# Kernel optimization log

Hardware: AMD Instinct MI355X
Metric: run time of the kernel (lower is better)

## Reference

```python
import jax, jax.numpy as jnp
import numpy as np

D_MODEL = 1024
NUM_HEADS = 16
D_K = D_MODEL // NUM_HEADS
B, S = 4, 2048


def setup_inputs() -> dict:
    key = jax.random.key(0)
    ks = jax.random.split(key, 12)
    scale = 1.0 / np.sqrt(D_MODEL)
    inp = {
        "query": jax.random.normal(ks[0], (B, S, D_MODEL), jnp.float32),
        "key": jax.random.normal(ks[1], (B, S, D_MODEL), jnp.float32),
        "value": jax.random.normal(ks[2], (B, S, D_MODEL), jnp.float32),
        # causal mask, broadcastable over (batch, heads)
        "mask": jnp.tril(jnp.ones((S, S), jnp.int32))[None, None, :, :],
        "Wq": jax.random.normal(ks[3], (D_MODEL, D_MODEL), jnp.float32) * scale,
        "bq": jnp.zeros((D_MODEL,), jnp.float32),
        "Wk": jax.random.normal(ks[4], (D_MODEL, D_MODEL), jnp.float32) * scale,
        "bk": jnp.zeros((D_MODEL,), jnp.float32),
        "Wv": jax.random.normal(ks[5], (D_MODEL, D_MODEL), jnp.float32) * scale,
        "bv": jnp.zeros((D_MODEL,), jnp.float32),
        "Wo": jax.random.normal(ks[6], (D_MODEL, D_MODEL), jnp.float32) * scale,
        "bo": jnp.zeros((D_MODEL,), jnp.float32),
    }
    return inp


def reference(query, key, value, mask, Wq, bq, Wk, bk, Wv, bv, Wo, bo):
    b = query.shape[0]
    # projections (torch Linear: x @ W.T + b)
    Q = query @ Wq.T + bq
    K = key @ Wk.T + bk
    V = value @ Wv.T + bv
    # [B, S, D] -> [B, H, S, d_k]
    def split_heads(x):
        return x.reshape(b, -1, NUM_HEADS, D_K).transpose(0, 2, 1, 3)
    Q, K, V = split_heads(Q), split_heads(K), split_heads(V)
    # scaled dot-product attention, full score matrix as in original
    scores = jnp.einsum("bhqd,bhkd->bhqk", Q, K) / jnp.sqrt(jnp.float32(D_K))
    scores = jnp.where(mask == 0, jnp.float32(-jnp.inf), scores)
    attn = jax.nn.softmax(scores, axis=-1)  # dropout p=0.0 -> identity
    x = jnp.einsum("bhqk,bhkd->bhqd", attn, V)
    # [B, H, S, d_k] -> [B, S, D]
    x = x.transpose(0, 2, 1, 3).reshape(b, -1, D_MODEL)
    return x @ Wo.T + bo
```

## Files before the change

kernel.cpp:

```cpp
#include <hip/hip_runtime.h>
#include <hip/hip_bf16.h>
#include <stdint.h>

#define D_MODEL 1024
#define NUM_HEADS 16
#define DK 64
#define BATCH 4
#define SEQ 2048
#define MTOT (BATCH * SEQ)

typedef unsigned short u16;
typedef unsigned int u32;
typedef __bf16 bf16x8 __attribute__((ext_vector_type(8)));
typedef float f32x4 __attribute__((ext_vector_type(4)));
typedef short s16x4 __attribute__((ext_vector_type(4)));
typedef int   i32x4 __attribute__((ext_vector_type(4)));
typedef int   i32x2 __attribute__((ext_vector_type(2)));
typedef uint  u32x2 __attribute__((ext_vector_type(2)));

__device__ __forceinline__ f32x4 mfma16(s16x4 a, s16x4 b, f32x4 c) {
  return __builtin_amdgcn_mfma_f32_16x16x16bf16_1k(a, b, c, 0, 0, 0);
}

__device__ __forceinline__ u16 f2bf(float f) {
  union { float f; unsigned u; } c; c.f = f;
  unsigned u = c.u + 0x7fffu + ((c.u >> 16) & 1u);
  return (u16)(u >> 16);
}
__device__ __forceinline__ u32 pack_bf2(float f0, float f1) {
  return __builtin_amdgcn_perm(__float_as_uint(f1), __float_as_uint(f0), 0x07060302u);
}
__device__ __forceinline__ s16x4 cast_s16x4(u32 lo, u32 hi) {
  u32x2 t = {lo, hi};
  return (s16x4)t;
}

__device__ __forceinline__ void async16(void* g, void* lds) {
  __builtin_amdgcn_global_load_lds(
      (__attribute__((address_space(1))) void*)g,
      (__attribute__((address_space(3))) void*)lds,
      16, 0, 0);
}

struct CvtArgs {
  const float* s[7];
  u16* d[7];
  int n[7];
};
__global__ __launch_bounds__(256)
void cvt_multi(CvtArgs a) {
  const int which = blockIdx.y;
  const int n = a.n[which];
  const int i = (blockIdx.x * 256 + threadIdx.x) * 8;
  if (i >= n) return;
  const float* s = a.s[which];
  u16* d = a.d[which];
  const float4 x = *(const float4*)(s + i);
  const float4 y = *(const float4*)(s + i + 4);
  *(ushort4*)(d + i)     = make_ushort4(f2bf(x.x), f2bf(x.y), f2bf(x.z), f2bf(x.w));
  *(ushort4*)(d + i + 4) = make_ushort4(f2bf(y.x), f2bf(y.y), f2bf(y.z), f2bf(y.w));
}

struct GBatch {
  const u16* A[3]; const u16* W[3]; const float* bias[3];
  void* C[3]; float osc[3]; int mode[3];
};
__global__ __launch_bounds__(256, 2)
void gemm_bt_bias(GBatch ga)
{
  __shared__ __align__(16) u16 smem[24576];
  const int z = blockIdx.z;
  const u16* __restrict__ A = ga.A[z];
  const u16* __restrict__ W = ga.W[z];
  const float* __restrict__ bias = ga.bias[z];
  void* __restrict__ Cv = ga.C[z];
  const float oscale = ga.osc[z];
  const int mode = ga.mode[z];

  const int t = threadIdx.x;
  const int w = t >> 6, l = t & 63;
  const int quad = l >> 4, lane16 = l & 15;
  const int m0 = blockIdx.x * 128;
  const int n0 = blockIdx.y * 128;
  const int wm = (w >> 1) * 64, wn = (w & 1) * 64;

  const int srow = t >> 2;
  const int scol = (t & 3) * 8;
  const u16* Ag = A + (long)(m0 + srow) * D_MODEL + scol;
  const u16* Wg = W + (long)(n0 + srow) * D_MODEL + scol;

  f32x4 acc[4][4] = {};

  auto stage = [&](int buf, int k0) {
    u16* As_ = smem + buf * 8192;
    u16* Bs_ = As_ + 4096;
    async16((void*)(Ag + k0), As_ + w * 512);
    async16((void*)(Ag + 64 * D_MODEL + k0), As_ + w * 512 + 2048);
    async16((void*)(Wg + k0), Bs_ + w * 512);
    async16((void*)(Wg + 64 * D_MODEL + k0), Bs_ + w * 512 + 2048);
  };
  auto compute = [&](int buf) {
    const u16* As_ = smem + buf * 8192;
    const u16* Bs_ = As_ + 4096;
    bf16x8 af[4], bfr[4];
#pragma unroll
    for (int i = 0; i < 4; ++i)
      af[i] = *(const bf16x8*)&As_[(wm + i * 16 + lane16) * 32 + quad * 8];
#pragma unroll
    for (int i = 0; i < 4; ++i)
      bfr[i] = *(const bf16x8*)&Bs_[(wn + i * 16 + lane16) * 32 + quad * 8];
#pragma unroll
    for (int i = 0; i < 4; ++i)
#pragma unroll
      for (int jn = 0; jn < 4; ++jn)
        acc[i][jn] = __builtin_amdgcn_mfma_f32_16x16x32_bf16(af[i], bfr[jn], acc[i][jn], 0, 0, 0);
  };

  stage(0, 0);
  stage(1, 32);
  asm volatile("s_waitcnt vmcnt(4)" ::: "memory");
  __builtin_amdgcn_s_barrier();
  __builtin_amdgcn_sched_barrier(0);

  int buf = 0;
#pragma unroll 1
  for (int c = 0; c < 32; ++c) {
    if (c + 2 < 32) stage((buf + 2 >= 3) ? buf - 1 : buf + 2, (c + 2) * 32);
    compute(buf);
    if (c < 30) {
      asm volatile("s_waitcnt vmcnt(4)" ::: "memory");
      __builtin_amdgcn_s_barrier();
      __builtin_amdgcn_sched_barrier(0);
    } else if (c == 30) {
      asm volatile("s_waitcnt vmcnt(0)" ::: "memory");
      __builtin_amdgcn_s_barrier();
      __builtin_amdgcn_sched_barrier(0);
    }
    buf = (buf + 1 == 3) ? 0 : buf + 1;
  }
  __syncthreads();

  if (mode == 1) {
    u16* T = smem;
#pragma unroll
    for (int jn = 0; jn < 4; ++jn) {
      const int col = wn + jn * 16 + lane16;
      const float bb = bias[n0 + col];
#pragma unroll
      for (int i = 0; i < 4; ++i) {
        const int rbase = wm + i * 16 + quad * 4;
#pragma unroll
        for (int r = 0; r < 4; ++r)
          T[col * 132 + rbase + r] = f2bf((acc[i][jn][r] + bb) * oscale);
      }
    }
    __syncthreads();
    const int bq = m0 >> 11, sbase = m0 & 2047;
    const int a = t & 31;
    const int keystart = ((a >> 3) * 32) + (((a & 7) >> 1) * 4) + ((a & 1) * 16);
    u16* orow = (u16*)Cv + ((long)bq * 1024 + n0) * SEQ + sbase + 4 * a;
#pragma unroll
    for (int pass = 0; pass < 16; ++pass) {
      const int dkl = (t >> 5) + 8 * pass;
      *(u32x2*)(orow + (long)dkl * SEQ) = *(const u32x2*)&T[dkl * 132 + keystart];
    }
  } else {
#pragma unroll
    for (int jn = 0; jn < 4; ++jn) {
      const int col = n0 + wn + jn * 16 + lane16;
      const float bb = bias[col];
#pragma unroll
      for (int i = 0; i < 4; ++i) {
        const int rbase = m0 + wm + i * 16 + quad * 4;
#pragma unroll
        for (int r = 0; r < 4; ++r) {
          const float v = (acc[i][jn][r] + bb) * oscale;
          if (mode == 2) ((float*)Cv)[(long)(rbase + r) * D_MODEL + col] = v;
          else           ((u16*)Cv)[(long)(rbase + r) * D_MODEL + col] = f2bf(v);
        }
      }
    }
  }
}

__global__ __launch_bounds__(256, 3)
void attn_causal(const u16* __restrict__ Q, const u16* __restrict__ K,
                 const u16* __restrict__ VtX, u16* __restrict__ O)
{
  __shared__ __align__(16) u16 Kb[2][32][64];
  __shared__ __align__(16) u16 Vb[2][64][32];
  const int t = threadIdx.x;
  const int w = t >> 6, l = t & 63;
  const int quad = l >> 4, lane16 = l & 15;

  const int lin = blockIdx.x;
  const int xcd = lin & 7;
  const int j = lin >> 3;
  const int bh = xcd * 8 + (j & 7);
  const int g = 15 - (j >> 3);
  const int b = bh >> 4, h = bh & 15;
  const int sw = 4 * g + w;
  const int cmax = 4 * g + 3;
  const int qbase = sw * 32;

  const long qkbase = (long)b * SEQ * D_MODEL + h * DK;

  bf16x8 qf[2][2];
#pragma unroll
  for (int qi = 0; qi < 2; ++qi)
#pragma unroll
    for (int ks = 0; ks < 2; ++ks)
      qf[qi][ks] = *(const bf16x8*)&Q[qkbase +
          (long)(qbase + qi * 16 + lane16) * D_MODEL + ks * 32 + quad * 8];

  const int krow = t >> 3, kc = t & 7;
  const char* Kgt = (const char*)(K + qkbase) + (long)krow * (D_MODEL * 2) + kc * 16;
  u16* KbD0 = &Kb[0][krow][(kc ^ (krow & 7)) * 8];
  u16* KbD1 = &Kb[1][krow][(kc ^ (krow & 7)) * 8];
  const int vrow = t >> 2, vc = t & 3;
  const char* Vgt = (const char*)(VtX + ((long)b * 1024 + h * 64) * SEQ) +
                    (long)vrow * (SEQ * 2) + vc * 16;
  u16* VbD0 = &Vb[0][vrow][(vc ^ (vrow & 3)) * 8];
  u16* VbD1 = &Vb[1][vrow][(vc ^ (vrow & 3)) * 8];

  f32x4 oacc[4][2] = {};
  float lsum[2] = {0.f, 0.f};

  auto body = [&](const u16 (*Kbuf)[64], const u16 (*Vbuf)[32], bool diag) {
    bf16x8 kf[2][2];
#pragma unroll
    for (int kt = 0; kt < 2; ++kt)
#pragma unroll
      for (int ks = 0; ks < 2; ++ks)
        kf[kt][ks] = *(const bf16x8*)
            &Kbuf[kt * 16 + lane16][(((ks * 4 + quad) ^ (lane16 & 7)) * 8)];
    i32x4 vfd[4];
#pragma unroll
    for (int d = 0; d < 4; ++d)
      vfd[d] = *(const i32x4*)
          &Vbuf[d * 16 + lane16][((quad ^ (lane16 & 3)) * 8)];

    f32x4 st[2][2] = {};
    __builtin_amdgcn_s_setprio(1);
#pragma unroll
    for (int kt = 0; kt < 2; ++kt)
#pragma unroll
      for (int qi = 0; qi < 2; ++qi)
#pragma unroll
        for (int ks = 0; ks < 2; ++ks)
          st[kt][qi] = __builtin_amdgcn_mfma_f32_16x16x32_bf16(kf[kt][ks], qf[qi][ks], st[kt][qi], 0, 0, 0);
    __builtin_amdgcn_s_setprio(0);

    u32 pb[2][2][2];
#pragma unroll
    for (int kt = 0; kt < 2; ++kt)
#pragma unroll
      for (int qi = 0; qi < 2; ++qi) {
        float pv[4];
#pragma unroll
        for (int r = 0; r < 4; ++r) {
          float p = __builtin_amdgcn_exp2f(st[kt][qi][r]);
          if (diag && (kt * 16 + quad * 4 + r > qi * 16 + lane16)) p = 0.f;
          pv[r] = p;
        }
        lsum[qi] += (pv[0] + pv[1]) + (pv[2] + pv[3]);
        pb[kt][qi][0] = pack_bf2(pv[0], pv[1]);
        pb[kt][qi][1] = pack_bf2(pv[2], pv[3]);
      }

    __builtin_amdgcn_s_setprio(1);
#pragma unroll
    for (int d = 0; d < 4; ++d) {
      const s16x4 va0 = cast_s16x4((u32)vfd[d].x, (u32)vfd[d].y);
      const s16x4 va1 = cast_s16x4((u32)vfd[d].z, (u32)vfd[d].w);
#pragma unroll
      for (int qi = 0; qi < 2; ++qi) {
        const s16x4 pb0 = cast_s16x4(pb[0][qi][0], pb[0][qi][1]);
        const s16x4 pb1 = cast_s16x4(pb[1][qi][0], pb[1][qi][1]);
        oacc[d][qi] = mfma16(va0, pb0, oacc[d][qi]);
        oacc[d][qi] = mfma16(va1, pb1, oacc[d][qi]);
      }
    }
    __builtin_amdgcn_s_setprio(0);
  };

  {
    i32x4 a0 = *(const i32x4*)(Kgt);
    i32x4 a1 = *(const i32x4*)(Vgt);
    *(i32x4*)KbD0 = a0;
    *(i32x4*)VbD0 = a1;
  }
  i32x4 gKA = *(const i32x4*)(Kgt + 65536);
  i32x4 gVA = *(const i32x4*)(Vgt + 64);
  i32x4 gKB = *(const i32x4*)(Kgt + 2 * 65536);
  i32x4 gVB = *(const i32x4*)(Vgt + 2 * 64);
  __syncthreads();

  for (int c = 0; c <= cmax; c += 2) {
    *(i32x4*)KbD1 = gKA;
    *(i32x4*)VbD1 = gVA;
    if (c + 3 <= cmax) {
      gKA = *(const i32x4*)(Kgt + (long)(c + 3) * 65536);
      gVA = *(const i32x4*)(Vgt + (long)(c + 3) * 64);
    }
    if (c <= sw) body(Kb[0], Vb[0], c == sw);
    __syncthreads();
    if (c + 2 <= cmax) {
      *(i32x4*)KbD0 = gKB;
      *(i32x4*)VbD0 = gVB;
      if (c + 4 <= cmax) {
        gKB = *(const i32x4*)(Kgt + (long)(c + 4) * 65536);
        gVB = *(const i32x4*)(Vgt + (long)(c + 4) * 64);
      }
    }
    if (c + 1 <= sw) body(Kb[1], Vb[1], (c + 1) == sw);
    __syncthreads();
  }

  float linv[2];
#pragma unroll
  for (int qi = 0; qi < 2; ++qi) {
    float v = lsum[qi];
    v += __shfl_xor(v, 16);
    v += __shfl_xor(v, 32);
    linv[qi] = 1.f / v;
  }

#pragma unroll
  for (int qi = 0; qi < 2; ++qi) {
    const long row = (long)b * SEQ + qbase + qi * 16 + lane16;
#pragma unroll
    for (int d = 0; d < 4; ++d) {
      const u32 p0 = ((u32)f2bf(oacc[d][qi][0] * linv[qi])) |
                     ((u32)f2bf(oacc[d][qi][1] * linv[qi]) << 16);
      const u32 p1 = ((u32)f2bf(oacc[d][qi][2] * linv[qi])) |
                     ((u32)f2bf(oacc[d][qi][3] * linv[qi]) << 16);
      u32x2 pk = {p0, p1};
      *(u32x2*)&O[row * D_MODEL + h * 64 + d * 16 + quad * 4] = pk;
    }
  }
}

extern "C" void kernel_launch(void* const* d_in, const int* in_sizes, int n_in,
                              void* d_out, int out_size, void* d_ws, size_t ws_size,
                              hipStream_t stream) {
  const float* q  = (const float*)d_in[0];
  const float* k  = (const float*)d_in[1];
  const float* v  = (const float*)d_in[2];
  const float* Wq = (const float*)d_in[4];
  const float* bq = (const float*)d_in[5];
  const float* Wk = (const float*)d_in[6];
  const float* bk = (const float*)d_in[7];
  const float* Wv = (const float*)d_in[8];
  const float* bv = (const float*)d_in[9];
  const float* Wo = (const float*)d_in[10];
  const float* bo = (const float*)d_in[11];
  float* out = (float*)d_out;

  const size_t NT = (size_t)MTOT * D_MODEL;
  const size_t NW = (size_t)D_MODEL * D_MODEL;

  u16* w0  = (u16*)d_ws;
  u16* qb  = w0;
  u16* kb  = w0 + NT;
  u16* vb  = w0 + 2 * NT;
  u16* Wqb = w0 + 3 * NT;
  u16* Wkb = Wqb + NW;
  u16* Wvb = Wqb + 2 * NW;
  u16* Wob = Wqb + 3 * NW;
  u16* Qp  = (u16*)d_out;
  u16* Kp  = (u16*)d_out + NT;
  u16* Vpt = qb;
  u16* Xp  = kb;

  const dim3 blk(256);

  CvtArgs ca;
  ca.s[0] = q;  ca.d[0] = qb;  ca.n[0] = (int)NT;
  ca.s[1] = k;  ca.d[1] = kb;  ca.n[1] = (int)NT;
  ca.s[2] = v;  ca.d[2] = vb;  ca.n[2] = (int)NT;
  ca.s[3] = Wq; ca.d[3] = Wqb; ca.n[3] = (int)NW;
  ca.s[4] = Wk; ca.d[4] = Wkb; ca.n[4] = (int)NW;
  ca.s[5] = Wv; ca.d[5] = Wvb; ca.n[5] = (int)NW;
  ca.s[6] = Wo; ca.d[6] = Wob; ca.n[6] = (int)NW;
  cvt_multi<<<dim3(4096, 7), blk, 0, stream>>>(ca);

  const float SC = 0.125f * 1.4426950408889634f;

  GBatch g1;
  g1.A[0] = qb; g1.W[0] = Wqb; g1.bias[0] = bq; g1.C[0] = Qp;  g1.osc[0] = SC;  g1.mode[0] = 0;
  g1.A[1] = kb; g1.W[1] = Wkb; g1.bias[1] = bk; g1.C[1] = Kp;  g1.osc[1] = 1.f; g1.mode[1] = 0;
  g1.A[2] = vb; g1.W[2] = Wvb; g1.bias[2] = bv; g1.C[2] = Vpt; g1.osc[2] = 1.f; g1.mode[2] = 1;
  gemm_bt_bias<<<dim3(MTOT / 128, D_MODEL / 128, 3), blk, 0, stream>>>(g1);

  const dim3 agrid(1024);
  attn_causal<<<agrid, blk, 0, stream>>>(Qp, Kp, Vpt, Xp);

  GBatch g2;
  for (int i = 0; i < 3; ++i) {
    g2.A[i] = Xp; g2.W[i] = Wob; g2.bias[i] = bo; g2.C[i] = out;
    g2.osc[i] = 1.f; g2.mode[i] = 2;
  }
  gemm_bt_bias<<<dim3(MTOT / 128, D_MODEL / 128, 1), blk, 0, stream>>>(g2);
}
```

Before: 312.3 us.

## Deepen GEMM prefetch to four LDS stages and template epilogue mode

The projection GEMM moves from a 3-buffer to a 4-buffer LDS ring, so three k-chunks are in flight ahead of compute, with the vmcnt waits adjusted to match. The epilogue mode becomes a template parameter so the branch and the per-z argument struct lookups are resolved at compile time. The three Q/K/V projections, previously one batched launch over blockIdx.z, are now split into three separate launches. LDS use per block grows from 48KB to 64KB, which may limit occupancy, and the split launches give up the single large grid plus add launch gaps.

```diff
diff --git a/kernel.cpp b/kernel.cpp
--- a/kernel.cpp
+++ b/kernel.cpp
@@ -61,22 +61,13 @@
   *(ushort4*)(d + i + 4) = make_ushort4(f2bf(y.x), f2bf(y.y), f2bf(y.z), f2bf(y.w));
 }
 
-struct GBatch {
-  const u16* A[3]; const u16* W[3]; const float* bias[3];
-  void* C[3]; float osc[3]; int mode[3];
-};
+template <int MODE>
 __global__ __launch_bounds__(256, 2)
-void gemm_bt_bias(GBatch ga)
+void gemm_bt_bias(const u16* __restrict__ A, const u16* __restrict__ W,
+                  const float* __restrict__ bias, void* __restrict__ Cv,
+                  float oscale)
 {
-  __shared__ __align__(16) u16 smem[24576];
-  const int z = blockIdx.z;
-  const u16* __restrict__ A = ga.A[z];
-  const u16* __restrict__ W = ga.W[z];
-  const float* __restrict__ bias = ga.bias[z];
-  void* __restrict__ Cv = ga.C[z];
-  const float oscale = ga.osc[z];
-  const int mode = ga.mode[z];
-
+  __shared__ __align__(16) u16 smem[32768];
   const int t = threadIdx.x;
   const int w = t >> 6, l = t & 63;
   const int quad = l >> 4, lane16 = l & 15;
@@ -118,29 +109,28 @@
 
   stage(0, 0);
   stage(1, 32);
-  asm volatile("s_waitcnt vmcnt(4)" ::: "memory");
+  stage(2, 64);
+  asm volatile("s_waitcnt vmcnt(8)" ::: "memory");
   __builtin_amdgcn_s_barrier();
   __builtin_amdgcn_sched_barrier(0);
 
   int buf = 0;
 #pragma unroll 1
   for (int c = 0; c < 32; ++c) {
-    if (c + 2 < 32) stage((buf + 2 >= 3) ? buf - 1 : buf + 2, (c + 2) * 32);
+    if (c + 3 < 32) stage((buf + 3) & 3, (c + 3) * 32);
     compute(buf);
-    if (c < 30) {
-      asm volatile("s_waitcnt vmcnt(4)" ::: "memory");
+    if (c < 31) {
+      if (c <= 28)      asm volatile("s_waitcnt vmcnt(8)" ::: "memory");
+      else if (c == 29) asm volatile("s_waitcnt vmcnt(4)" ::: "memory");
+      else              asm volatile("s_waitcnt vmcnt(0)" ::: "memory");
       __builtin_amdgcn_s_barrier();
       __builtin_amdgcn_sched_barrier(0);
-    } else if (c == 30) {
-      asm volatile("s_waitcnt vmcnt(0)" ::: "memory");
-      __builtin_amdgcn_s_barrier();
-      __builtin_amdgcn_sched_barrier(0);
-    }
-    buf = (buf + 1 == 3) ? 0 : buf + 1;
+    }
+    buf = (buf + 1) & 3;
   }
   __syncthreads();
 
-  if (mode == 1) {
+  if constexpr (MODE == 1) {
     u16* T = smem;
 #pragma unroll
     for (int jn = 0; jn < 4; ++jn) {
@@ -175,7 +165,7 @@
 #pragma unroll
         for (int r = 0; r < 4; ++r) {
           const float v = (acc[i][jn][r] + bb) * oscale;
-          if (mode == 2) ((float*)Cv)[(long)(rbase + r) * D_MODEL + col] = v;
+          if (MODE == 2) ((float*)Cv)[(long)(rbase + r) * D_MODEL + col] = v;
           else           ((u16*)Cv)[(long)(rbase + r) * D_MODEL + col] = f2bf(v);
         }
       }
@@ -386,20 +376,14 @@
   cvt_multi<<<dim3(4096, 7), blk, 0, stream>>>(ca);
 
   const float SC = 0.125f * 1.4426950408889634f;
-
-  GBatch g1;
-  g1.A[0] = qb; g1.W[0] = Wqb; g1.bias[0] = bq; g1.C[0] = Qp;  g1.osc[0] = SC;  g1.mode[0] = 0;
-  g1.A[1] = kb; g1.W[1] = Wkb; g1.bias[1] = bk; g1.C[1] = Kp;  g1.osc[1] = 1.f; g1.mode[1] = 0;
-  g1.A[2] = vb; g1.W[2] = Wvb; g1.bias[2] = bv; g1.C[2] = Vpt; g1.osc[2] = 1.f; g1.mode[2] = 1;
-  gemm_bt_bias<<<dim3(MTOT / 128, D_MODEL / 128, 3), blk, 0, stream>>>(g1);
+  const dim3 ggrid(MTOT / 128, D_MODEL / 128);
+
+  gemm_bt_bias<0><<<ggrid, blk, 0, stream>>>(qb, Wqb, bq, Qp,  SC);
+  gemm_bt_bias<0><<<ggrid, blk, 0, stream>>>(kb, Wkb, bk, Kp,  1.f);
+  gemm_bt_bias<1><<<ggrid, blk, 0, stream>>>(vb, Wvb, bv, Vpt, 1.f);
 
   const dim3 agrid(1024);
   attn_causal<<<agrid, blk, 0, stream>>>(Qp, Kp, Vpt, Xp);
 
-  GBatch g2;
-  for (int i = 0; i < 3; ++i) {
-    g2.A[i] = Xp; g2.W[i] = Wob; g2.bias[i] = bo; g2.C[i] = out;
-    g2.osc[i] = 1.f; g2.mode[i] = 2;
-  }
-  gemm_bt_bias<<<dim3(MTOT / 128, D_MODEL / 128, 1), blk, 0, stream>>>(g2);
-}
+  gemm_bt_bias<2><<<ggrid, blk, 0, stream>>>(Xp, Wob, bo, out, 1.f);
+}
```

Result: no change. 313.6 us (+0.4%).
